# Kernel optimization log

Measured on AMD Instinct MI355X. Metric: run time of the kernel, lower is better.

The kernel has to match this reference:

```python
import jax, jax.numpy as jnp
import numpy as np
import math

# init config (matches init_kwargs); sigma/alpha are squared in __init__
SIGMA2 = 8.0 ** 2
ALPHA2 = 8.0 ** 2
C_SIZE = 512
STRIDE = 8
MINX = 1e-06
M = 100                      # ratio=100 > 1 -> M = int(ratio), capped at 100
K = C_SIZE // STRIDE         # 64 grid cells per axis
G = K * K                    # 4096 density-field cells
B, N = 8, 512                # images, annotated points per image
TWO_PI = 2.0 * math.pi


def setup_inputs():
    key = jax.random.key(0)
    k1, _ = jax.random.split(key)
    points = jax.random.uniform(k1, (B, N, 2), dtype=jnp.float32) * C_SIZE
    st_sizes = jnp.full((B,), float(C_SIZE), dtype=jnp.float32)
    return {"points": points, "st_sizes": st_sizes}


def _per_image(pts, cood):
    # pts: [N,2]; cood: [K]
    x = pts[:, 0]
    y = pts[:, 1]
    dx = x[:, None] - cood[None, :]                 # [N,K]
    dy = y[:, None] - cood[None, :]                 # [N,K]
    # dis_all = y_dis[:, :, None] + x_dis[:, None, :] flattened: g = iy*K + ix
    dis = (dy[:, :, None] ** 2 + dx[:, None, :] ** 2).reshape(pts.shape[0], G)  # [N,G]
    s1 = ALPHA2 + SIGMA2
    s2 = ALPHA2 + SIGMA2 / 2.0
    m = jnp.exp(-0.5 / s1 * dis) / (TWO_PI * s1)    # [N,G]
    tv = jnp.exp(-0.5 / s2 * dis) / (TWO_PI * s2)
    v = (tv / (TWO_PI * 2.0 * SIGMA2)).sum(0) - (m ** 2).sum(0)   # [G] (sel_v == v, no bg)
    # top-M cells by sel_v, then sort indices ascending (ratio>1 branch -> static M)
    inds = jnp.argsort(-v)
    Minds = jnp.sort(inds[:M])                      # [M]
    v = jnp.maximum(v, MINX)                        # add=False -> clamp
    # xf[n, iy*K+ix] = x_n - cood[ix]; yf[n, iy*K+ix] = y_n - cood[iy]
    iy = Minds // K
    ix = Minds % K
    xfM = dx[:, ix]                                 # [N,M]
    yfM = dy[:, iy]                                 # [N,M]
    df = (xfM[:, None, :] - xfM[:, :, None]) ** 2 + (yfM[:, None, :] - yfM[:, :, None]) ** 2
    af = (0.5 * (xfM[:, None, :] + xfM[:, :, None])) ** 2 + (0.5 * (yfM[:, None, :] + yfM[:, :, None])) ** 2
    g1 = jnp.exp(-0.5 / (2.0 * SIGMA2) * df) / (TWO_PI * 2.0 * SIGMA2)          # [N,M,M]
    tmpv2 = (g1 * (jnp.exp(-0.5 / s2 * af) / (TWO_PI * s2))).sum(0) + g1.sum(0)  # [M,M]
    disM = dis[:, Minds]                            # [N,M]
    tmpm2 = jnp.exp(-0.5 / s1 * disM) / (TWO_PI * s1)
    A = tmpv2 - tmpm2.T @ tmpm2                     # [M,M]
    eye = jnp.eye(M, dtype=bool)
    A = jnp.where(eye, 1e-10, A)                    # diag overwritten to 1e-10
    vM = v[Minds] + 1e-10
    tmpA = vM[:, None] * jnp.linalg.inv(A) * vM[None, :] + jnp.diag(vM)
    Bm = jnp.linalg.inv(tmpA)
    return m, v, A, Bm, Minds


def reference(points, st_sizes):
    # st_sizes only matters for use_background=True; kept for signature fidelity
    cood = jnp.arange(0, C_SIZE, STRIDE, dtype=jnp.float32) + STRIDE / 2.0
    m, v, A, Bm, Minds = jax.vmap(lambda p: _per_image(p, cood))(points)
    return m, v, A, Bm, Minds
```

## Files before the change

kernel.cpp:

```cpp
#include <hip/hip_runtime.h>
#include <math.h>

#ifndef M_PI
#define M_PI 3.14159265358979323846
#endif

#define BB 8
#define NN 512
#define KK 64
#define GG 4096
#define MM 100

#define SZ_VD    (BB*GG*4u)
#define OFF_VD   0u
#define SZ_VM    (BB*MM*4u)
#define OFF_VM   (OFF_VD + SZ_VD)
#define SZ_AD    (BB*MM*MM*4u)
#define OFF_AD   (OFF_VM + SZ_VM)

#define OUT_M  0
#define OUT_V  (BB*NN*GG)
#define OUT_A  (OUT_V + BB*GG)
#define OUT_B  (OUT_A + BB*MM*MM)
#define OUT_MI (OUT_B + BB*MM*MM)

#define MU_PER 8
#define MU_VP 4096
#define MU_AS 2048
#define MU_IV 10240

__device__ __forceinline__ void m_units(const float* __restrict__ pts,
                                        float* __restrict__ out, int u0, int cnt) {
  const float CM = (float)(1.0/(2.0*M_PI*128.0));
  for (int k = 0; k < cnt; ++k) {
    int u = u0 + k;
    int t = u*256 + (int)threadIdx.x;
    int e = t << 2;
    int img = e >> 21;
    int rem = e & ((1 << 21) - 1);
    int n = rem >> 12;
    int g = rem & 4095;
    int iy = g >> 6, ix = g & 63;
    float x = pts[(img*NN + n)*2 + 0];
    float y = pts[(img*NN + n)*2 + 1];
    float dy = y - (8.0f*iy + 4.0f);
    float ey = __expf(dy*dy*(-0.5f/128.0f));
    float4 r;
    float dx0 = x - (8.0f*ix + 4.0f);
    float dx1 = x - (8.0f*(ix+1) + 4.0f);
    float dx2 = x - (8.0f*(ix+2) + 4.0f);
    float dx3 = x - (8.0f*(ix+3) + 4.0f);
    r.x = ey*__expf(dx0*dx0*(-0.5f/128.0f))*CM;
    r.y = ey*__expf(dx1*dx1*(-0.5f/128.0f))*CM;
    r.z = ey*__expf(dx2*dx2*(-0.5f/128.0f))*CM;
    r.w = ey*__expf(dx3*dx3*(-0.5f/128.0f))*CM;
    *reinterpret_cast<float4*>(&out[OUT_M + e]) = r;
  }
}

__device__ __forceinline__ float flt_readlane(float v, int l) {
  return __int_as_float(__builtin_amdgcn_readlane(__float_as_int(v), l));
}

__global__ __launch_bounds__(256) void k_vpart(const float* __restrict__ pts,
                                               float* __restrict__ vd,
                                               float* __restrict__ out) {
  __shared__ double sEy2[16][66], sEx2[16][66], sEy3[16][66], sEx3[16][66];
  __shared__ float px[NN], py[NN];
  int bid = blockIdx.x;
  if (bid >= BB*16) { m_units(pts, out, (bid - BB*16)*MU_PER, MU_PER); return; }
  int tile = bid & 15;
  int img = bid >> 4;
  int iy0 = (tile >> 2) << 4;
  int ix0 = (tile & 3) << 4;
  int tx = threadIdx.x & 15, ty = threadIdx.x >> 4;
  for (int s = threadIdx.x; s < NN; s += 256) {
    px[s] = pts[(img*NN + s)*2 + 0];
    py[s] = pts[(img*NN + s)*2 + 1];
  }
  double aV = 0.0, aM = 0.0;
  for (int kc = 0; kc < 8; ++kc) {
    int nb = kc << 6;
    __syncthreads();
    for (int s = threadIdx.x; s < 16*64; s += 256) {
      int row = s >> 6, n = s & 63;
      int nn = nb + n;
      double y = (double)py[nn];
      double cy = 8.0*(iy0 + row) + 4.0;
      double dy = y - cy, dy2 = dy*dy;
      sEy2[row][n] = exp(dy2*(-0.5/96.0));
      sEy3[row][n] = exp(dy2*(-1.0/128.0));
      double x = (double)px[nn];
      double cx = 8.0*(ix0 + row) + 4.0;
      double dx = x - cx, dx2 = dx*dx;
      sEx2[row][n] = exp(dx2*(-0.5/96.0));
      sEx3[row][n] = exp(dx2*(-1.0/128.0));
    }
    __syncthreads();
    #pragma unroll 8
    for (int n = 0; n < 64; ++n) {
      aV += sEy2[ty][n]*sEx2[tx][n];
      aM += sEy3[ty][n]*sEx3[tx][n];
    }
  }
  const double CTV = 1.0/((2.0*M_PI*96.0)*(2.0*M_PI*128.0));
  const double CM2 = 1.0/((2.0*M_PI*128.0)*(2.0*M_PI*128.0));
  vd[img*GG + (iy0 + ty)*KK + ix0 + tx] = (float)(CTV*aV - CM2*aM);
}

union AselU {
  struct {
    unsigned int ku[GG];
    unsigned int hist4[4][256];
    unsigned int wq[4];
    unsigned int sPref, sMask;
    unsigned int sRem, sPickB, sPickRem, sCGt, sCEq;
    int tie[128];
  } se;
  struct {
    float sxi[16][130], syi[16][130], sti[16][130];
    float sxj[16][130], syj[16][130], stj[16][130];
    float px[NN], py[NN];
    float cxi[16], cyi[16], cxj[16], cyj[16];
  } ka;
};

__device__ __forceinline__ void bitonic128(int* a, int tid) {
  for (int kk = 2; kk <= 128; kk <<= 1)
    for (int jj = kk >> 1; jj > 0; jj >>= 1) {
      if (tid < 128) {
        int p = tid ^ jj;
        if (p > tid) {
          int x = a[tid], y = a[p];
          bool up = ((tid & kk) == 0);
          if (up ? (x > y) : (x < y)) { a[tid] = y; a[p] = x; }
        }
      }
      __syncthreads();
    }
}

__global__ __launch_bounds__(256) void k_Asel(const float* __restrict__ pts,
                                              const float* __restrict__ vd,
                                              float* __restrict__ out,
                                              float* __restrict__ ad,
                                              float* __restrict__ vm) {
  __shared__ AselU u;
  __shared__ int selFinal[128];
  int bid = blockIdx.x;
  if (bid >= BB*28) { m_units(pts, out, MU_VP + (bid - BB*28)*MU_PER, MU_PER); return; }
  int img = bid / 28;
  int tile = bid - img*28;
  bool tile0 = (tile == 0);
  int tid = threadIdx.x;
  int wv = tid >> 6;
  int lane = tid & 63;

  for (int t = 0; t < 16; ++t) {
    int g = t*256 + tid;
    float v = vd[img*GG + g];
    if (tile0) out[OUT_V + img*GG + g] = fmaxf(v, 1e-6f);
    int w = __float_as_int(v);
    u.se.ku[g] = (w < 0) ? ~(unsigned)w : ((unsigned)w | 0x80000000u);
  }
  if (tid == 0) {
    u.se.sRem = 100; u.se.sPref = 0u; u.se.sMask = 0u;
    u.se.sCGt = 0; u.se.sCEq = 0;
  }
  for (int shift = 24; shift >= 0; shift -= 8) {
    for (int c = 0; c < 4; ++c) u.se.hist4[c][tid] = 0;
    __syncthreads();
    unsigned mask = u.se.sMask, pref = u.se.sPref;
    for (int t = 0; t < 16; ++t) {
      unsigned k = u.se.ku[t*256 + tid];
      if ((k & mask) == pref)
        atomicAdd(&u.se.hist4[wv][(k >> shift) & 255u], 1u);
    }
    __syncthreads();
    unsigned tot = u.se.hist4[0][tid] + u.se.hist4[1][tid]
                 + u.se.hist4[2][tid] + u.se.hist4[3][tid];
    unsigned val = tot;
    #pragma unroll
    for (int off = 1; off < 64; off <<= 1) {
      unsigned o = (unsigned)__shfl_down((int)val, off);
      if (lane + off < 64) val += o;
    }
    if (lane == 0) u.se.wq[wv] = val;
    __syncthreads();
    unsigned suf = val;
    for (int w2 = wv + 1; w2 < 4; ++w2) suf += u.se.wq[w2];
    unsigned rem = u.se.sRem;
    unsigned sgt = suf - tot;
    if (suf >= rem && sgt < rem) { u.se.sPickB = (unsigned)tid; u.se.sPickRem = rem - sgt; }
    __syncthreads();
    if (tid == 0) {
      u.se.sPref |= u.se.sPickB << shift;
      u.se.sMask |= 255u << shift;
      u.se.sRem   = u.se.sPickRem;
    }
    __syncthreads();
  }
  unsigned T = u.se.sPref;
  for (int t = 0; t < 16; ++t) {
    int g = t*256 + tid;
    unsigned k = u.se.ku[g];
    if (k > T) {
      unsigned p = atomicAdd(&u.se.sCGt, 1u);
      selFinal[p] = g;
    } else if (k == T) {
      unsigned p = atomicAdd(&u.se.sCEq, 1u);
      if (p < 128) u.se.tie[p] = g;
    }
  }
  __syncthreads();
  unsigned cgt = u.se.sCGt, ceq = u.se.sCEq, r = u.se.sRem;
  if (tid < 128 && tid >= (int)((ceq < 128u) ? ceq : 128u)) u.se.tie[tid] = 0x7fffffff;
  __syncthreads();
  bitonic128(u.se.tie, tid);
  if (tid < (int)r) selFinal[cgt + tid] = u.se.tie[tid];
  if (tid >= MM && tid < 128) selFinal[tid] = 0x7fffffff;
  __syncthreads();
  bitonic128(selFinal, tid);
  if (tile0 && tid < MM) {
    int mi = selFinal[tid];
    out[OUT_MI + img*MM + tid] = (float)mi;
    vm[img*MM + tid] = fmaxf(vd[img*GG + mi], 1e-6f) + 1e-10f;
  }
  __syncthreads();

  int it = 0, trem = tile;
  while (trem >= 7 - it) { trem -= 7 - it; ++it; }
  int jt = it + trem;
  int i0 = it*16, j0 = jt*16;
  int tj = tid & 15, ti = tid >> 4;
  int i = i0 + ti, j = j0 + tj;
  const float CM = (float)(1.0/(2.0*M_PI*128.0));
  const float C1 = (float)(1.0/(2.0*M_PI*128.0));
  const float C2 = (float)(1.0/(2.0*M_PI*96.0));
  for (int s = tid; s < NN; s += 256) {
    u.ka.px[s] = pts[(img*NN + s)*2 + 0];
    u.ka.py[s] = pts[(img*NN + s)*2 + 1];
  }
  if (tid < 16) {
    int gi = i0 + tid; if (gi > 99) gi = 99;
    int mi = selFinal[gi];
    u.ka.cxi[tid] = 8.0f*(mi & 63) + 4.0f;
    u.ka.cyi[tid] = 8.0f*(mi >> 6) + 4.0f;
  } else if (tid < 32) {
    int rr = tid - 16;
    int gj = j0 + rr; if (gj > 99) gj = 99;
    int mj = selFinal[gj];
    u.ka.cxj[rr] = 8.0f*(mj & 63) + 4.0f;
    u.ka.cyj[rr] = 8.0f*(mj >> 6) + 4.0f;
  }
  float aV = 0.0f, aM = 0.0f;
  for (int nc = 0; nc < NN; nc += 128) {
    __syncthreads();
    for (int s = tid; s < 16*128; s += 256) {
      int row = s >> 7, n = s & 127;
      float x = u.ka.px[nc + n], y = u.ka.py[nc + n];
      float fxi = x - u.ka.cxi[row], fyi = y - u.ka.cyi[row];
      u.ka.sxi[row][n] = fxi; u.ka.syi[row][n] = fyi;
      u.ka.sti[row][n] = __expf((fxi*fxi + fyi*fyi)*(-0.5f/128.0f))*CM;
      float fxj = x - u.ka.cxj[row], fyj = y - u.ka.cyj[row];
      u.ka.sxj[row][n] = fxj; u.ka.syj[row][n] = fyj;
      u.ka.stj[row][n] = __expf((fxj*fxj + fyj*fyj)*(-0.5f/128.0f))*CM;
    }
    __syncthreads();
    #pragma unroll 4
    for (int n = 0; n < 128; ++n) {
      float xi = u.ka.sxi[ti][n], yi = u.ka.syi[ti][n], tii = u.ka.sti[ti][n];
      float xj = u.ka.sxj[tj][n], yj = u.ka.syj[tj][n], tjj = u.ka.stj[tj][n];
      float ddx = xj - xi, ddy = yj - yi;
      float df = ddx*ddx + ddy*ddy;
      float sx = 0.5f*(xi + xj), sy = 0.5f*(yi + yj);
      float af = sx*sx + sy*sy;
      float g1 = __expf(df*(-0.5f/128.0f))*C1;
      float h  = __expf(af*(-0.5f/96.0f))*C2;
      aV += g1 + g1*h;
      aM += tii*tjj;
    }
  }
  if (i < 100 && j < 100) {
    float val = (i == j) ? 1e-10f : (float)((double)aV - (double)aM);
    out[OUT_A + (img*MM + i)*MM + j] = val;
    ad[(img*MM + i)*MM + j] = val;
    if (it != jt) {
      out[OUT_A + (img*MM + j)*MM + i] = val;
      ad[(img*MM + j)*MM + i] = val;
    }
  }
}

__global__ __launch_bounds__(256)
void k_inv_m(const float* __restrict__ ad,
             const float* __restrict__ vm,
             const float* __restrict__ pts,
             float* __restrict__ out) {
  __shared__ float S[128*17];
  __shared__ float Pr[16*113];
  __shared__ float svm[112];
  if (blockIdx.x >= BB) {
    m_units(pts, out, MU_VP + MU_AS + ((int)blockIdx.x - BB)*MU_PER, MU_PER);
    return;
  }
  int img = blockIdx.x;
  int tx = threadIdx.x & 15, ty = threadIdx.x >> 4;
  float C[7][7];
  if (threadIdx.x < 100) svm[threadIdx.x] = vm[img*MM + threadIdx.x];
  #pragma unroll
  for (int a = 0; a < 7; ++a) {
    int r = ty + 16*a;
    #pragma unroll
    for (int b = 0; b < 7; ++b) {
      int j = tx + 16*b;
      float v2 = (r < 100 && j < 100) ? ad[(img*MM + r)*MM + j] : 0.0f;
      if (r == j && r < 100) v2 += vm[img*MM + r];
      C[a][b] = v2;
    }
  }
  for (int p = 0; p < 7; ++p) {
    int k0 = p*16;
    int nbp = (p == 6) ? 4 : 16;
    #pragma unroll
    for (int a = 0; a < 7; ++a) {
      int r = ty + 16*a;
      float val = 0.0f;
      #pragma unroll
      for (int b = 0; b < 7; ++b) if (b == p) val = C[a][b];
      S[r*17 + tx] = (r < 100 && tx < nbp) ? val : 0.0f;
    }
    {
      float pv[7];
      #pragma unroll
      for (int b = 0; b < 7; ++b) pv[b] = 0.0f;
      #pragma unroll
      for (int a = 0; a < 7; ++a) {
        #pragma unroll
        for (int b = 0; b < 7; ++b) if (a == p) pv[b] = C[a][b];
      }
      #pragma unroll
      for (int b = 0; b < 7; ++b) Pr[ty*113 + tx + 16*b] = pv[b];
    }
    __syncthreads();
    if (threadIdx.x < 64) {
      int lane = threadIdx.x;
      float P0[16], P1[16];
      #pragma unroll
      for (int c = 0; c < 16; ++c) {
        P0[c] = S[lane*17 + c];
        P1[c] = (lane + 64 < 112) ? S[(lane + 64)*17 + c] : 0.0f;
      }
      #pragma unroll
      for (int kk = 0; kk < 16; ++kk) {
        if (kk < nbp) {
          int kg = k0 + kk;
          int r1 = lane + 64;
          bool khigh = kg >= 64; int kl = kg & 63;
          float pivinv = 1.0f / flt_readlane(khigh ? P1[kk] : P0[kk], kl);
          float pr[16];
          #pragma unroll
          for (int c = 0; c < 16; ++c) {
            float pv = flt_readlane(khigh ? P1[c] : P0[c], kl);
            pr[c] = (c == kk) ? pivinv : pv*pivinv;
          }
          {
            float f = P0[kk];
            if (lane == kg) {
              #pragma unroll
              for (int c = 0; c < 16; ++c) P0[c] = pr[c];
            } else {
              #pragma unroll
              for (int c = 0; c < 16; ++c) P0[c] = ((c == kk) ? 0.0f : P0[c]) - f*pr[c];
            }
          }
          {
            float f = P1[kk];
            if (r1 == kg) {
              #pragma unroll
              for (int c = 0; c < 16; ++c) P1[c] = pr[c];
            } else {
              #pragma unroll
              for (int c = 0; c < 16; ++c) P1[c] = ((c == kk) ? 0.0f : P1[c]) - f*pr[c];
            }
          }
        }
      }
      #pragma unroll
      for (int c = 0; c < 16; ++c) {
        S[lane*17 + c] = P0[c];
        if (lane + 64 < 112) S[(lane + 64)*17 + c] = P1[c];
      }
    }
    __syncthreads();
    #pragma unroll
    for (int a = 0; a < 7; ++a) {
      int r = ty + 16*a;
      bool prow_ = (r >= k0) && (r < k0 + 16);
      #pragma unroll
      for (int b = 0; b < 7; ++b) {
        if (r >= 100 || b == p || prow_) C[a][b] = 0.0f;
      }
    }
    #pragma unroll 4
    for (int t = 0; t < 16; ++t) {
      bool tok = (t < nbp);
      float bt[7], sa[7];
      #pragma unroll
      for (int b = 0; b < 7; ++b) bt[b] = tok ? Pr[t*113 + tx + 16*b] : 0.0f;
      #pragma unroll
      for (int a = 0; a < 7; ++a) sa[a] = S[(ty + 16*a)*17 + t];
      #pragma unroll
      for (int a = 0; a < 7; ++a)
        #pragma unroll
        for (int b = 0; b < 7; ++b) C[a][b] += sa[a]*bt[b];
    }
    #pragma unroll
    for (int a = 0; a < 7; ++a) {
      int r = ty + 16*a;
      float sval = S[r*17 + tx];
      #pragma unroll
      for (int b = 0; b < 7; ++b) if (b == p) C[a][b] = sval;
    }
    __syncthreads();
  }
  #pragma unroll
  for (int a = 0; a < 7; ++a) {
    int r = ty + 16*a; if (r >= 100) continue;
    float dinv = 1.0f / svm[r];
    #pragma unroll
    for (int b = 0; b < 7; ++b) {
      int c = tx + 16*b; if (c >= 100) continue;
      float val = ((c == r) ? dinv : 0.0f) - C[a][b];
      out[OUT_B + (img*MM + r)*MM + c] = val;
    }
  }
}

extern "C" void kernel_launch(void* const* d_in, const int* in_sizes, int n_in,
                              void* d_out, int out_size, void* d_ws, size_t ws_size,
                              hipStream_t stream) {
  const float* pts = (const float*)d_in[0];
  float* out = (float*)d_out;
  char* ws = (char*)d_ws;
  float* vd  = (float*)(ws + OFF_VD);
  float* vmd = (float*)(ws + OFF_VM);
  float* ad  = (float*)(ws + OFF_AD);

  hipLaunchKernelGGL(k_vpart, dim3(BB*16 + MU_VP/MU_PER), dim3(256), 0, stream, pts, vd, out);
  hipLaunchKernelGGL(k_Asel, dim3(BB*28 + MU_AS/MU_PER), dim3(256), 0, stream, pts, vd, out, ad, vmd);
  hipLaunchKernelGGL(k_inv_m, dim3(BB + MU_IV/MU_PER), dim3(256), 0, stream, ad, vmd, pts, out);
}
```

Before: 211.8 us.

## Split point sum across two blocks and compute Gaussian tables by exponential recurrence

The v-partial kernel now splits the 512 points into two halves handled by separate blocks, writing double partials that the selection kernel sums. This doubles the block count and so improves occupancy. Gaussian table rows are no longer one double exp per entry: each thread computes two exps and walks the 16 grid rows by multiplicative recurrence (E*=R, R*=Q). This removes most double-precision exp calls, at some risk of error accumulation across the recurrence, and adds a doubled workspace and extra reads in k_Asel.

```diff
diff --git a/kernel.cpp b/kernel.cpp
--- a/kernel.cpp
+++ b/kernel.cpp
@@ -11,7 +11,7 @@
 #define GG 4096
 #define MM 100
 
-#define SZ_VD    (BB*GG*4u)
+#define SZ_VD    (BB*GG*8u*2u)
 #define OFF_VD   0u
 #define SZ_VM    (BB*MM*4u)
 #define OFF_VM   (OFF_VD + SZ_VD)
@@ -63,49 +63,56 @@
 }
 
 __global__ __launch_bounds__(256) void k_vpart(const float* __restrict__ pts,
-                                               float* __restrict__ vd,
+                                               double* __restrict__ vd,
                                                float* __restrict__ out) {
-  __shared__ double sEy2[16][66], sEx2[16][66], sEy3[16][66], sEx3[16][66];
-  __shared__ float px[NN], py[NN];
+  __shared__ double sEy2[16][66], sEy3[16][66], sEx2[16][66], sEx3[16][66];
+  __shared__ float px[256], py[256];
   int bid = blockIdx.x;
-  if (bid >= BB*16) { m_units(pts, out, (bid - BB*16)*MU_PER, MU_PER); return; }
-  int tile = bid & 15;
-  int img = bid >> 4;
+  if (bid >= BB*32) { m_units(pts, out, (bid - BB*32)*MU_PER, MU_PER); return; }
+  int half = bid & 1;
+  int rem = bid >> 1;
+  int tile = rem & 15;
+  int img = rem >> 4;
   int iy0 = (tile >> 2) << 4;
   int ix0 = (tile & 3) << 4;
   int tx = threadIdx.x & 15, ty = threadIdx.x >> 4;
-  for (int s = threadIdx.x; s < NN; s += 256) {
-    px[s] = pts[(img*NN + s)*2 + 0];
-    py[s] = pts[(img*NN + s)*2 + 1];
-  }
+  int n = threadIdx.x & 63;
+  int tbl = threadIdx.x >> 6;
+  for (int s = threadIdx.x; s < 256; s += 256) {
+    px[s] = pts[(img*NN + half*256 + s)*2 + 0];
+    py[s] = pts[(img*NN + half*256 + s)*2 + 1];
+  }
+  const double alpha = (tbl & 1) ? (1.0/128.0) : (0.5/96.0);
+  const double Q = exp(-128.0*alpha);
+  const int base = (tbl >= 2) ? ix0 : iy0;
+  double* dst = (tbl == 0) ? &sEy2[0][0] : (tbl == 1) ? &sEy3[0][0]
+              : (tbl == 2) ? &sEx2[0][0] : &sEx3[0][0];
   double aV = 0.0, aM = 0.0;
-  for (int kc = 0; kc < 8; ++kc) {
-    int nb = kc << 6;
-    __syncthreads();
-    for (int s = threadIdx.x; s < 16*64; s += 256) {
-      int row = s >> 6, n = s & 63;
-      int nn = nb + n;
-      double y = (double)py[nn];
-      double cy = 8.0*(iy0 + row) + 4.0;
-      double dy = y - cy, dy2 = dy*dy;
-      sEy2[row][n] = exp(dy2*(-0.5/96.0));
-      sEy3[row][n] = exp(dy2*(-1.0/128.0));
-      double x = (double)px[nn];
-      double cx = 8.0*(ix0 + row) + 4.0;
-      double dx = x - cx, dx2 = dx*dx;
-      sEx2[row][n] = exp(dx2*(-0.5/96.0));
-      sEx3[row][n] = exp(dx2*(-1.0/128.0));
+  for (int kc = 0; kc < 4; ++kc) {
+    int nbl = kc << 6;
+    __syncthreads();
+    {
+      int nn = nbl + n;
+      double coord = (tbl >= 2) ? (double)px[nn] : (double)py[nn];
+      double d0 = coord - (8.0*base + 4.0);
+      double E = exp(-alpha*d0*d0);
+      double R = exp(alpha*(16.0*d0 - 64.0));
+      #pragma unroll
+      for (int row = 0; row < 16; ++row) {
+        dst[row*66 + n] = E;
+        E *= R; R *= Q;
+      }
     }
     __syncthreads();
     #pragma unroll 8
-    for (int n = 0; n < 64; ++n) {
-      aV += sEy2[ty][n]*sEx2[tx][n];
-      aM += sEy3[ty][n]*sEx3[tx][n];
+    for (int n2 = 0; n2 < 64; ++n2) {
+      aV += sEy2[ty][n2]*sEx2[tx][n2];
+      aM += sEy3[ty][n2]*sEx3[tx][n2];
     }
   }
   const double CTV = 1.0/((2.0*M_PI*96.0)*(2.0*M_PI*128.0));
   const double CM2 = 1.0/((2.0*M_PI*128.0)*(2.0*M_PI*128.0));
-  vd[img*GG + (iy0 + ty)*KK + ix0 + tx] = (float)(CTV*aV - CM2*aM);
+  vd[half*(BB*GG) + img*GG + (iy0 + ty)*KK + ix0 + tx] = CTV*aV - CM2*aM;
 }
 
 union AselU {
@@ -141,7 +148,7 @@
 }
 
 __global__ __launch_bounds__(256) void k_Asel(const float* __restrict__ pts,
-                                              const float* __restrict__ vd,
+                                              const double* __restrict__ vd,
                                               float* __restrict__ out,
                                               float* __restrict__ ad,
                                               float* __restrict__ vm) {
@@ -158,7 +165,7 @@
 
   for (int t = 0; t < 16; ++t) {
     int g = t*256 + tid;
-    float v = vd[img*GG + g];
+    float v = (float)(vd[img*GG + g] + vd[BB*GG + img*GG + g]);
     if (tile0) out[OUT_V + img*GG + g] = fmaxf(v, 1e-6f);
     int w = __float_as_int(v);
     u.se.ku[g] = (w < 0) ? ~(unsigned)w : ((unsigned)w | 0x80000000u);
@@ -224,7 +231,8 @@
   if (tile0 && tid < MM) {
     int mi = selFinal[tid];
     out[OUT_MI + img*MM + tid] = (float)mi;
-    vm[img*MM + tid] = fmaxf(vd[img*GG + mi], 1e-6f) + 1e-10f;
+    float vsel = (float)(vd[img*GG + mi] + vd[BB*GG + img*GG + mi]);
+    vm[img*MM + tid] = fmaxf(vsel, 1e-6f) + 1e-10f;
   }
   __syncthreads();
 
@@ -443,11 +451,11 @@
   const float* pts = (const float*)d_in[0];
   float* out = (float*)d_out;
   char* ws = (char*)d_ws;
-  float* vd  = (float*)(ws + OFF_VD);
+  double* vd  = (double*)(ws + OFF_VD);
   float* vmd = (float*)(ws + OFF_VM);
   float* ad  = (float*)(ws + OFF_AD);
 
-  hipLaunchKernelGGL(k_vpart, dim3(BB*16 + MU_VP/MU_PER), dim3(256), 0, stream, pts, vd, out);
+  hipLaunchKernelGGL(k_vpart, dim3(BB*32 + MU_VP/MU_PER), dim3(256), 0, stream, pts, vd, out);
   hipLaunchKernelGGL(k_Asel, dim3(BB*28 + MU_AS/MU_PER), dim3(256), 0, stream, pts, vd, out, ad, vmd);
   hipLaunchKernelGGL(k_inv_m, dim3(BB + MU_IV/MU_PER), dim3(256), 0, stream, ad, vmd, pts, out);
 }
```

Result: faster. 201.4 us (-4.9%).
